# Performance work log

Hardware: AMD Instinct MI355X
Metric: run time of the kernel (lower is better)

The kernel has to match this reference:

```python
import jax, jax.numpy as jnp
import numpy as np

EPS = 1e-5


def setup_inputs() -> dict:
    key = jax.random.key(0)
    ks = jax.random.split(key, 10)
    B, C, H, W = 8, 128, 64, 64
    inputs = jax.random.normal(ks[0], (B, C, H, W), dtype=jnp.float32)
    # GroupNorm affine params
    gn_w = jnp.ones((C,), dtype=jnp.float32)
    gn_b = jnp.zeros((C,), dtype=jnp.float32)
    # Linear layers: torch nn.Linear weight is [out, in]
    s = 1.0 / np.sqrt(C)
    Wq = jax.random.uniform(ks[1], (C, C), jnp.float32, -s, s)
    bq = jax.random.uniform(ks[2], (C,), jnp.float32, -s, s)
    Wk = jax.random.uniform(ks[3], (C, C), jnp.float32, -s, s)
    bk = jax.random.uniform(ks[4], (C,), jnp.float32, -s, s)
    Wv = jax.random.uniform(ks[5], (C, C), jnp.float32, -s, s)
    bv = jax.random.uniform(ks[6], (C,), jnp.float32, -s, s)
    Wp = jax.random.uniform(ks[7], (C, C), jnp.float32, -s, s)
    bp = jax.random.uniform(ks[8], (C,), jnp.float32, -s, s)
    return {"inputs": inputs, "gn_w": gn_w, "gn_b": gn_b,
            "Wq": Wq, "bq": bq, "Wk": Wk, "bk": bk,
            "Wv": Wv, "bv": bv, "Wp": Wp, "bp": bp,
            "groups": 32}


def _group_norm(x, w, b, groups):
    B, C, H, W = x.shape
    xg = x.reshape(B, groups, C // groups, H, W)
    mu = jnp.mean(xg, axis=(2, 3, 4), keepdims=True)
    var = jnp.var(xg, axis=(2, 3, 4), keepdims=True)
    xn = ((xg - mu) * jax.lax.rsqrt(var + EPS)).reshape(B, C, H, W)
    return xn * w[None, :, None, None] + b[None, :, None, None]


def reference(inputs, gn_w, gn_b, Wq, bq, Wk, bk, Wv, bv, Wp, bp, groups):
    B, C, H, W = inputs.shape
    scale = C ** (-0.5)
    normed = _group_norm(inputs, gn_w, gn_b, groups)  # [B,C,H,W]
    x = normed.transpose(0, 2, 3, 1).reshape(B, H * W, C)  # [B,N,C] tokens
    q = x @ Wq.T + bq
    k = x @ Wk.T + bk
    v = x @ Wv.T + bv
    # full dense attention over N = H*W tokens, single head
    scores = jnp.einsum('bnc,bmc->bnm', q, k) * scale  # [B,N,N]
    attn = jax.nn.softmax(scores, axis=-1)
    out = jnp.einsum('bnm,bmc->bnc', attn, v)
    proj = out @ Wp.T + bp
    proj = proj.reshape(B, H, W, C).transpose(0, 3, 1, 2)
    return normed + proj
```

## Files before the change

### kernel.cpp

```cpp
#include <hip/hip_runtime.h>
#include <hip/hip_bf16.h>
#include <math.h>

typedef __bf16 bf16_t;
typedef __bf16 bf16x8 __attribute__((ext_vector_type(8)));
typedef float  f32x4  __attribute__((ext_vector_type(4)));
typedef float  f32x16 __attribute__((ext_vector_type(16)));

#define BB 8
#define CC 128
#define NN 4096
#define LDP 136
#define SCALE2 0.12751743342f

static __device__ __forceinline__ f32x4 mfma16(bf16x8 a, bf16x8 b, f32x4 c) {
    return __builtin_amdgcn_mfma_f32_16x16x32_bf16(a, b, c, 0, 0, 0);
}
static __device__ __forceinline__ f32x16 mfma32(bf16x8 a, bf16x8 b, f32x16 c) {
    return __builtin_amdgcn_mfma_f32_32x32x16_bf16(a, b, c, 0, 0, 0);
}
static __device__ __forceinline__ void gld16(const void* g, void* l) {
    __builtin_amdgcn_global_load_lds(
        (const __attribute__((address_space(1))) void*)g,
        (__attribute__((address_space(3))) void*)l, 16, 0, 0);
}
static __device__ __forceinline__ unsigned pack2bf(float a, float b) {
    union { bf16_t h[2]; unsigned u; } r;
    r.h[0] = (bf16_t)a; r.h[1] = (bf16_t)b;
    return r.u;
}

__global__ void __launch_bounds__(256) gn_stats(const float* __restrict__ in,
                                                float* __restrict__ stats) {
    int bg = blockIdx.x;
    const float4* p4 = (const float4*)(in + (size_t)bg * 16384);
    int tid = threadIdx.x;
    float s = 0.f, ss = 0.f;
    for (int i = tid; i < 4096; i += 256) {
        float4 v = p4[i];
        s  += v.x + v.y + v.z + v.w;
        ss += v.x*v.x + v.y*v.y + v.z*v.z + v.w*v.w;
    }
    for (int off = 1; off < 64; off <<= 1) {
        s  += __shfl_xor(s,  off, 64);
        ss += __shfl_xor(ss, off, 64);
    }
    __shared__ float red[8];
    int wv = tid >> 6;
    if ((tid & 63) == 0) { red[wv*2] = s; red[wv*2+1] = ss; }
    __syncthreads();
    if (tid == 0) {
        float S  = red[0]+red[2]+red[4]+red[6];
        float SS = red[1]+red[3]+red[5]+red[7];
        float mu  = S * (1.f/16384.f);
        float var = SS * (1.f/16384.f) - mu*mu;
        stats[bg*2]   = mu;
        stats[bg*2+1] = rsqrtf(var + 1e-5f);
    }
}

__global__ void __launch_bounds__(256) gn_apply(const float* __restrict__ in,
                                                const float* __restrict__ gw,
                                                const float* __restrict__ gb,
                                                const float* __restrict__ stats,
                                                float* __restrict__ normed,
                                                bf16_t* __restrict__ x) {
    int b  = blockIdx.x >> 6;
    int p0 = (blockIdx.x & 63) << 6;
    int tid = threadIdx.x;
    __shared__ bf16_t tile[64 * 130];
    for (int i = tid; i < 8192; i += 256) {
        int c = i >> 6, p = i & 63;
        size_t idx = ((size_t)(b*CC + c)) * NN + p0 + p;
        float v = in[idx];
        int sg = b*32 + (c >> 2);
        float xn = (v - stats[sg*2]) * stats[sg*2+1] * gw[c] + gb[c];
        normed[idx] = xn;
        tile[p*130 + c] = (bf16_t)xn;
    }
    __syncthreads();
    bf16_t* xb = x + ((size_t)(b*NN + p0)) * CC;
    for (int i = tid; i < 4096; i += 256) {
        int p = i >> 6, cp = i & 63;
        unsigned int d = *(const unsigned int*)&tile[p*130 + cp*2];
        *(unsigned int*)&xb[p*CC + cp*2] = d;
    }
}

__global__ void __launch_bounds__(256) qkv_gemm(const bf16_t* __restrict__ x,
        const float* __restrict__ Wq, const float* __restrict__ bq,
        const float* __restrict__ Wk, const float* __restrict__ bk,
        const float* __restrict__ Wv, const float* __restrict__ bv,
        bf16_t* __restrict__ q, bf16_t* __restrict__ k, bf16_t* __restrict__ vT) {
    __shared__ bf16_t wb[CC * LDP];
    const int ph  = blockIdx.x >> 8;
    const int blk = blockIdx.x & 255;
    int b  = blk >> 5;
    int n0 = (blk & 31) << 7;
    int tid = threadIdx.x;
    int lane = tid & 63, l15 = lane & 15, quad = lane >> 4;
    int w = tid >> 6;
    bf16x8 afr[2][4];
    #pragma unroll
    for (int rt = 0; rt < 2; rt++)
        #pragma unroll
        for (int kb = 0; kb < 4; kb++)
            afr[rt][kb] = *(const bf16x8*)&x[(size_t)(b*NN + n0 + w*32 + rt*16 + l15)*CC + kb*32 + quad*8];

    const float* W  = (ph == 0) ? Wq : (ph == 1 ? Wk : Wv);
    const float* bs = (ph == 0) ? bq : (ph == 1 ? bk : bv);
    for (int i = tid; i < 2048; i += 256) {
        int row = i >> 4, s8 = i & 15;
        const float* wp = W + row*128 + s8*8;
        bf16x8 v;
        #pragma unroll
        for (int j = 0; j < 8; j++) v[j] = (bf16_t)wp[j];
        *(bf16x8*)&wb[row*LDP + s8*8] = v;
    }
    __syncthreads();
    f32x4 acc[2][8];
    f32x4 z = {0.f, 0.f, 0.f, 0.f};
    #pragma unroll
    for (int rt = 0; rt < 2; rt++)
        #pragma unroll
        for (int t = 0; t < 8; t++) acc[rt][t] = z;
    #pragma unroll
    for (int kb = 0; kb < 4; kb++)
        #pragma unroll
        for (int t = 0; t < 8; t++) {
            bf16x8 bf = *(const bf16x8*)&wb[(t*16 + l15)*LDP + kb*32 + quad*8];
            acc[0][t] = mfma16(afr[0][kb], bf, acc[0][t]);
            acc[1][t] = mfma16(afr[1][kb], bf, acc[1][t]);
        }
    __syncthreads();
    if (ph < 2) {
        float sc = (ph == 0) ? SCALE2 : 1.0f;
        #pragma unroll
        for (int t = 0; t < 8; t++) {
            float bias = bs[t*16 + l15];
            #pragma unroll
            for (int rt = 0; rt < 2; rt++)
                #pragma unroll
                for (int r = 0; r < 4; r++) {
                    int nloc = w*32 + rt*16 + quad*4 + r;
                    wb[nloc*LDP + t*16 + l15] = (bf16_t)((acc[rt][t][r] + bias) * sc);
                }
        }
        __syncthreads();
        bf16_t* outp = (ph == 0) ? q : k;
        for (int i = tid; i < 2048; i += 256) {
            int row = i >> 4, g = i & 15;
            bf16x8 vv = *(const bf16x8*)&wb[row*LDP + g*8];
            int gd = (ph == 0) ? g : (g ^ (row & 15));
            *(bf16x8*)&outp[(size_t)(b*NN + n0 + row)*CC + gd*8] = vv;
        }
    } else {
        #pragma unroll
        for (int t = 0; t < 8; t++) {
            float bias = bs[t*16 + l15];
            #pragma unroll
            for (int rt = 0; rt < 2; rt++)
                #pragma unroll
                for (int r = 0; r < 4; r++) {
                    int nloc = w*32 + rt*16 + quad*4 + r;
                    wb[(t*16 + l15)*LDP + nloc] = (bf16_t)(acc[rt][t][r] + bias);
                }
        }
        __syncthreads();
        for (int i = tid; i < 8192; i += 256) {
            int c = i >> 6, np = i & 63;
            unsigned int d = *(const unsigned int*)&wb[c*LDP + np*2];
            int npp = (np & ~6) | ((np & 2) << 1) | ((np & 4) >> 1);
            int g = (npp >> 2) ^ (c & 15);
            *(unsigned int*)&vT[(size_t)(b*CC + c)*NN + n0 + (g << 3) + ((npp & 3) << 1)] = d;
        }
    }
}

__global__ void __launch_bounds__(512, 2) flash_attn(const bf16_t* __restrict__ qg_,
                                                     const bf16_t* __restrict__ kg,
                                                     const bf16_t* __restrict__ vg,
                                                     unsigned* __restrict__ opd,
                                                     float* __restrict__ mlf) {
    __shared__ bf16_t kbuf[2][128*128];
    __shared__ bf16_t vbuf[2][128*128];
    const int b    = blockIdx.x >> 5;
    const int qb   = (blockIdx.x >> 1) & 15;
    const int jh   = blockIdx.x & 1;
    const int q0   = qb << 8;
    const int j00  = jh << 11;
    const int tid  = threadIdx.x;
    const int lane = tid & 63;
    const int l31  = lane & 31;
    const int h    = lane >> 5;
    const int w    = tid >> 6;

    bf16x8 qf[8];
    {
        const bf16_t* qr = qg_ + ((size_t)(b*NN + q0 + w*32 + l31))*CC + h*8;
        #pragma unroll
        for (int kc = 0; kc < 8; kc++) qf[kc] = *(const bf16x8*)(qr + kc*16);
    }
    int gofs[8];
    #pragma unroll
    for (int kc = 0; kc < 8; kc++) gofs[kc] = ((2*kc + h) ^ (l31 & 15)) << 3;

    f32x16 ot[4];
    #pragma unroll
    for (int ct = 0; ct < 4; ct++)
        #pragma unroll
        for (int r = 0; r < 16; r++) ot[ct][r] = 0.f;
    float l = 0.f;

    {
        const bf16_t* kt = kg + ((size_t)(b*NN + j00))*CC;
        #pragma unroll
        for (int it = 0; it < 4; it++) {
            int cb = it*512 + tid;
            gld16(kt + (size_t)cb*8, &kbuf[0][cb*8]);
        }
        #pragma unroll
        for (int it = 0; it < 4; it++) {
            int c = it*512 + tid;
            gld16(vg + ((size_t)(b*CC + (c >> 4)))*NN + j00 + (c & 15)*8, &vbuf[0][c*8]);
        }
    }
    __syncthreads();

    for (int i = 0; i < 16; i++) {
        const int cur = i & 1;
        if (i < 15) {
            const int j0n = j00 + ((i + 1) << 7);
            const bf16_t* kt = kg + ((size_t)(b*NN + j0n))*CC;
            #pragma unroll
            for (int it = 0; it < 4; it++) {
                int cb = it*512 + tid;
                gld16(kt + (size_t)cb*8, &kbuf[cur^1][cb*8]);
            }
            #pragma unroll
            for (int it = 0; it < 4; it++) {
                int c = it*512 + tid;
                gld16(vg + ((size_t)(b*CC + (c >> 4)))*NN + j0n + (c & 15)*8, &vbuf[cur^1][c*8]);
            }
        }
        #pragma unroll
        for (int tt = 0; tt < 4; tt++) {
            f32x16 st;
            #pragma unroll
            for (int r = 0; r < 16; r++) st[r] = 0.f;
            const bf16_t* krow = &kbuf[cur][(tt*32 + l31)*128];
            #pragma unroll
            for (int kc = 0; kc < 8; kc++) {
                bf16x8 kf = *(const bf16x8*)(krow + gofs[kc]);
                st = mfma32(kf, qf[kc], st);
            }
            #pragma unroll
            for (int r = 0; r < 16; r++) st[r] = __builtin_amdgcn_exp2f(st[r]);
            {
                float a0 = (st[0]+st[1]) + (st[2]+st[3]);
                float a1 = (st[4]+st[5]) + (st[6]+st[7]);
                float a2 = (st[8]+st[9]) + (st[10]+st[11]);
                float a3 = (st[12]+st[13]) + (st[14]+st[15]);
                l += (a0 + a1) + (a2 + a3);
            }
            union { unsigned u[4]; bf16x8 v; } pf[2];
            #pragma unroll
            for (int kcl = 0; kcl < 2; kcl++)
                #pragma unroll
                for (int g = 0; g < 4; g++)
                    pf[kcl].u[g] = pack2bf(st[8*kcl + 2*g], st[8*kcl + 2*g + 1]);
            #pragma unroll
            for (int kcl = 0; kcl < 2; kcl++) {
                const int kc = tt*2 + kcl;
                #pragma unroll
                for (int ct = 0; ct < 4; ct++) {
                    bf16x8 vf = *(const bf16x8*)&vbuf[cur][(ct*32 + l31)*128 + gofs[kc]];
                    ot[ct] = mfma32(vf, pf[kcl].v, ot[ct]);
                }
            }
        }
        __syncthreads();
    }
    l += __shfl_xor(l, 32, 64);
    const int row0 = q0 + w*32 + l31;
    unsigned* ob = opd + ((size_t)(jh*BB + b)) * 64 * NN;
    #pragma unroll
    for (int ct = 0; ct < 4; ct++)
        #pragma unroll
        for (int rp = 0; rp < 8; rp++) {
            int cpair = ct*16 + (rp & 1) + 4*(rp >> 1) + 2*h;
            ob[(size_t)cpair*NN + row0] = pack2bf(ot[ct][2*rp], ot[ct][2*rp + 1]);
        }
    if (h == 0)
        mlf[((size_t)(jh*BB + b))*NN + row0] = l;
}

__global__ void __launch_bounds__(256) merge_attn(const unsigned* __restrict__ opd,
                                                  const float* __restrict__ mlf,
                                                  bf16_t* __restrict__ ao) {
    __shared__ float inv[128];
    __shared__ unsigned tile[128 * 65];
    const int b  = blockIdx.x >> 5;
    const int q0 = (blockIdx.x & 31) << 7;
    const int tid = threadIdx.x;
    if (tid < 128) {
        float lt = 0.f;
        #pragma unroll
        for (int p = 0; p < 2; p++) lt += mlf[((size_t)(p*BB + b))*NN + q0 + tid];
        inv[tid] = 1.0f / lt;
    }
    __syncthreads();
    for (int i = tid; i < 8192; i += 256) {
        int q = i & 127, cp = i >> 7;
        float lo = 0.f, hi = 0.f;
        #pragma unroll
        for (int p = 0; p < 2; p++) {
            unsigned u = opd[(((size_t)(p*BB + b))*64 + cp)*NN + q0 + q];
            union { unsigned u; float f; } a, c;
            a.u = u << 16; c.u = u & 0xffff0000u;
            lo += a.f; hi += c.f;
        }
        float s = inv[q];
        tile[q*65 + cp] = pack2bf(lo * s, hi * s);
    }
    __syncthreads();
    unsigned* aod = (unsigned*)ao;
    for (int i = tid; i < 8192; i += 256) {
        int q = i >> 6, cp = i & 63;
        aod[((size_t)(b*NN + q0 + q))*64 + cp] = tile[q*65 + cp];
    }
}

__global__ void __launch_bounds__(256) proj_out(const bf16_t* __restrict__ ao,
                                                const float* __restrict__ Wp,
                                                const float* __restrict__ bp,
                                                float* __restrict__ out) {
    __shared__ bf16_t wb[CC * LDP];
    int b  = blockIdx.x >> 5;
    int n0 = (blockIdx.x & 31) << 7;
    int tid = threadIdx.x;
    int lane = tid & 63, l15 = lane & 15, quad = lane >> 4;
    int w = tid >> 6;
    bf16x8 afr[2][4];
    #pragma unroll
    for (int rt = 0; rt < 2; rt++)
        #pragma unroll
        for (int kb = 0; kb < 4; kb++)
            afr[rt][kb] = *(const bf16x8*)&ao[(size_t)(b*NN + n0 + w*32 + rt*16 + l15)*CC + kb*32 + quad*8];
    for (int i = tid; i < 2048; i += 256) {
        int row = i >> 4, s8 = i & 15;
        const float* wp = Wp + row*128 + s8*8;
        bf16x8 v;
        #pragma unroll
        for (int j = 0; j < 8; j++) v[j] = (bf16_t)wp[j];
        *(bf16x8*)&wb[row*LDP + s8*8] = v;
    }
    __syncthreads();
    f32x4 acc[2][8];
    f32x4 z = {0.f, 0.f, 0.f, 0.f};
    #pragma unroll
    for (int rt = 0; rt < 2; rt++)
        #pragma unroll
        for (int t = 0; t < 8; t++) acc[rt][t] = z;
    #pragma unroll
    for (int kb = 0; kb < 4; kb++)
        #pragma unroll
        for (int t = 0; t < 8; t++) {
            bf16x8 bf = *(const bf16x8*)&wb[(t*16 + l15)*LDP + kb*32 + quad*8];
            acc[0][t] = mfma16(afr[0][kb], bf, acc[0][t]);
            acc[1][t] = mfma16(afr[1][kb], bf, acc[1][t]);
        }
    __syncthreads();
    #pragma unroll
    for (int t = 0; t < 8; t++) {
        float bias = bp[t*16 + l15];
        #pragma unroll
        for (int rt = 0; rt < 2; rt++)
            #pragma unroll
            for (int r = 0; r < 4; r++) {
                int nloc = w*32 + rt*16 + quad*4 + r;
                wb[(t*16 + l15)*LDP + nloc] = (bf16_t)(acc[rt][t][r] + bias);
            }
    }
    __syncthreads();
    for (int i = tid; i < 8192; i += 256) {
        int c = i >> 6, np = i & 63;
        bf16_t b0 = wb[c*LDP + np*2], b1 = wb[c*LDP + np*2 + 1];
        size_t idx = (size_t)(b*CC + c)*NN + n0 + np*2;
        float2 nv = *(float2*)&out[idx];
        nv.x += (float)b0;
        nv.y += (float)b1;
        *(float2*)&out[idx] = nv;
    }
}

extern "C" void kernel_launch(void* const* d_in, const int* in_sizes, int n_in,
                              void* d_out, int out_size, void* d_ws, size_t ws_size,
                              hipStream_t stream) {
    const float* in = (const float*)d_in[0];
    const float* gw = (const float*)d_in[1];
    const float* gb = (const float*)d_in[2];
    const float* Wq = (const float*)d_in[3];
    const float* bq = (const float*)d_in[4];
    const float* Wk = (const float*)d_in[5];
    const float* bk = (const float*)d_in[6];
    const float* Wv = (const float*)d_in[7];
    const float* bv = (const float*)d_in[8];
    const float* Wp = (const float*)d_in[9];
    const float* bp = (const float*)d_in[10];
    float* out = (float*)d_out;

    char* ws = (char*)d_ws;
    const size_t SZ = (size_t)BB * NN * CC * 2;
    float*    stats = (float*)ws;
    bf16_t*   x  = (bf16_t*)(ws + 2048);
    bf16_t*   q  = (bf16_t*)(ws + 2048 + SZ);
    bf16_t*   kk = (bf16_t*)(ws + 2048 + 2*SZ);
    bf16_t*   vT = (bf16_t*)(ws + 2048 + 3*SZ);
    bf16_t*   ao = (bf16_t*)(ws + 2048 + 4*SZ);
    unsigned* op = (unsigned*)(ws + 2048 + 5*SZ);
    float*    ml = (float*)(ws + 2048 + 5*SZ + (size_t)2*BB*64*NN*4);

    gn_stats  <<<256, 256, 0, stream>>>(in, stats);
    gn_apply  <<<512, 256, 0, stream>>>(in, gw, gb, stats, out, x);
    qkv_gemm  <<<768, 256, 0, stream>>>(x, Wq, bq, Wk, bk, Wv, bv, q, kk, vT);
    flash_attn<<<256, 512, 0, stream>>>(q, kk, vT, op, ml);
    merge_attn<<<256, 256, 0, stream>>>(op, ml, ao);
    proj_out  <<<256, 256, 0, stream>>>(ao, Wp, bp, out);
}
```

Baseline: 201.6 us.

## Fuse groupnorm apply into QKV GEMM, merge into projection, split KV into quarters

Group-norm application moves into the QKV GEMM, which now reads the fp32 input and builds the bf16 token tile in shared memory. The split-KV merge moves into the projection kernel, which also recomputes the normalized residual from the input. Flash attention now splits keys into four chunks of 1024 using 64-key tiles, giving 512 blocks with a launch bound allowing 4 blocks per CU. This removes two launches and the x/ao round trips through global memory. In exchange the GN math is recomputed three times (once per Q/K/V phase), and the partial-output traffic to merge doubles.

```diff
diff --git a/kernel.cpp b/kernel.cpp
--- a/kernel.cpp
+++ b/kernel.cpp
@@ -59,40 +59,14 @@
     }
 }
 
-__global__ void __launch_bounds__(256) gn_apply(const float* __restrict__ in,
-                                                const float* __restrict__ gw,
-                                                const float* __restrict__ gb,
-                                                const float* __restrict__ stats,
-                                                float* __restrict__ normed,
-                                                bf16_t* __restrict__ x) {
-    int b  = blockIdx.x >> 6;
-    int p0 = (blockIdx.x & 63) << 6;
-    int tid = threadIdx.x;
-    __shared__ bf16_t tile[64 * 130];
-    for (int i = tid; i < 8192; i += 256) {
-        int c = i >> 6, p = i & 63;
-        size_t idx = ((size_t)(b*CC + c)) * NN + p0 + p;
-        float v = in[idx];
-        int sg = b*32 + (c >> 2);
-        float xn = (v - stats[sg*2]) * stats[sg*2+1] * gw[c] + gb[c];
-        normed[idx] = xn;
-        tile[p*130 + c] = (bf16_t)xn;
-    }
-    __syncthreads();
-    bf16_t* xb = x + ((size_t)(b*NN + p0)) * CC;
-    for (int i = tid; i < 4096; i += 256) {
-        int p = i >> 6, cp = i & 63;
-        unsigned int d = *(const unsigned int*)&tile[p*130 + cp*2];
-        *(unsigned int*)&xb[p*CC + cp*2] = d;
-    }
-}
-
-__global__ void __launch_bounds__(256) qkv_gemm(const bf16_t* __restrict__ x,
+__global__ void __launch_bounds__(256) qkv_gemm(const float* __restrict__ in,
+        const float* __restrict__ stats, const float* __restrict__ gw, const float* __restrict__ gb,
         const float* __restrict__ Wq, const float* __restrict__ bq,
         const float* __restrict__ Wk, const float* __restrict__ bk,
         const float* __restrict__ Wv, const float* __restrict__ bv,
         bf16_t* __restrict__ q, bf16_t* __restrict__ k, bf16_t* __restrict__ vT) {
     __shared__ bf16_t wb[CC * LDP];
+    __shared__ bf16_t xt[128 * 130];
     const int ph  = blockIdx.x >> 8;
     const int blk = blockIdx.x & 255;
     int b  = blk >> 5;
@@ -100,13 +74,19 @@
     int tid = threadIdx.x;
     int lane = tid & 63, l15 = lane & 15, quad = lane >> 4;
     int w = tid >> 6;
-    bf16x8 afr[2][4];
-    #pragma unroll
-    for (int rt = 0; rt < 2; rt++)
-        #pragma unroll
-        for (int kb = 0; kb < 4; kb++)
-            afr[rt][kb] = *(const bf16x8*)&x[(size_t)(b*NN + n0 + w*32 + rt*16 + l15)*CC + kb*32 + quad*8];
-
+
+    for (int i = tid; i < 4096; i += 256) {
+        int c = i >> 5, p4 = i & 31;
+        const float4* inp = (const float4*)(in + (size_t)(b*CC + c)*NN + n0);
+        float4 v = inp[p4];
+        int sg = b*32 + (c >> 2);
+        float mu = stats[sg*2], rs = stats[sg*2+1];
+        float gwc = gw[c], gbc = gb[c];
+        xt[(p4*4 + 0)*130 + c] = (bf16_t)((v.x - mu)*rs*gwc + gbc);
+        xt[(p4*4 + 1)*130 + c] = (bf16_t)((v.y - mu)*rs*gwc + gbc);
+        xt[(p4*4 + 2)*130 + c] = (bf16_t)((v.z - mu)*rs*gwc + gbc);
+        xt[(p4*4 + 3)*130 + c] = (bf16_t)((v.w - mu)*rs*gwc + gbc);
+    }
     const float* W  = (ph == 0) ? Wq : (ph == 1 ? Wk : Wv);
     const float* bs = (ph == 0) ? bq : (ph == 1 ? bk : bv);
     for (int i = tid; i < 2048; i += 256) {
@@ -118,6 +98,12 @@
         *(bf16x8*)&wb[row*LDP + s8*8] = v;
     }
     __syncthreads();
+    bf16x8 afr[2][4];
+    #pragma unroll
+    for (int rt = 0; rt < 2; rt++)
+        #pragma unroll
+        for (int kb = 0; kb < 4; kb++)
+            afr[rt][kb] = *(const bf16x8*)&xt[(w*32 + rt*16 + l15)*130 + kb*32 + quad*8];
     f32x4 acc[2][8];
     f32x4 z = {0.f, 0.f, 0.f, 0.f};
     #pragma unroll
@@ -171,24 +157,26 @@
             int c = i >> 6, np = i & 63;
             unsigned int d = *(const unsigned int*)&wb[c*LDP + np*2];
             int npp = (np & ~6) | ((np & 2) << 1) | ((np & 4) >> 1);
-            int g = (npp >> 2) ^ (c & 15);
-            *(unsigned int*)&vT[(size_t)(b*CC + c)*NN + n0 + (g << 3) + ((npp & 3) << 1)] = d;
-        }
-    }
-}
-
-__global__ void __launch_bounds__(512, 2) flash_attn(const bf16_t* __restrict__ qg_,
+            int g128 = npp >> 2, s = npp & 3;
+            int jblk = g128 >> 3, g64 = g128 & 7;
+            int gs = g64 ^ (c & 7);
+            *(unsigned int*)&vT[(size_t)(b*CC + c)*NN + n0 + jblk*64 + (gs << 3) + (s << 1)] = d;
+        }
+    }
+}
+
+__global__ void __launch_bounds__(512, 4) flash_attn(const bf16_t* __restrict__ qg_,
                                                      const bf16_t* __restrict__ kg,
                                                      const bf16_t* __restrict__ vg,
                                                      unsigned* __restrict__ opd,
                                                      float* __restrict__ mlf) {
-    __shared__ bf16_t kbuf[2][128*128];
-    __shared__ bf16_t vbuf[2][128*128];
-    const int b    = blockIdx.x >> 5;
-    const int qb   = (blockIdx.x >> 1) & 15;
-    const int jh   = blockIdx.x & 1;
+    __shared__ bf16_t kbuf[2][64*128];
+    __shared__ bf16_t vbuf[2][128*64];
+    const int b    = blockIdx.x >> 6;
+    const int qb   = (blockIdx.x >> 2) & 15;
+    const int jq   = blockIdx.x & 3;
     const int q0   = qb << 8;
-    const int j00  = jh << 11;
+    const int j00  = jq << 10;
     const int tid  = threadIdx.x;
     const int lane = tid & 63;
     const int l31  = lane & 31;
@@ -201,9 +189,12 @@
         #pragma unroll
         for (int kc = 0; kc < 8; kc++) qf[kc] = *(const bf16x8*)(qr + kc*16);
     }
-    int gofs[8];
-    #pragma unroll
-    for (int kc = 0; kc < 8; kc++) gofs[kc] = ((2*kc + h) ^ (l31 & 15)) << 3;
+    int gofs16[8];
+    #pragma unroll
+    for (int kc = 0; kc < 8; kc++) gofs16[kc] = ((2*kc + h) ^ (l31 & 15)) << 3;
+    int gofs8[4];
+    #pragma unroll
+    for (int kc = 0; kc < 4; kc++) gofs8[kc] = ((2*kc + h) ^ (l31 & 7)) << 3;
 
     f32x16 ot[4];
     #pragma unroll
@@ -215,14 +206,15 @@
     {
         const bf16_t* kt = kg + ((size_t)(b*NN + j00))*CC;
         #pragma unroll
-        for (int it = 0; it < 4; it++) {
-            int cb = it*512 + tid;
-            gld16(kt + (size_t)cb*8, &kbuf[0][cb*8]);
-        }
-        #pragma unroll
-        for (int it = 0; it < 4; it++) {
-            int c = it*512 + tid;
-            gld16(vg + ((size_t)(b*CC + (c >> 4)))*NN + j00 + (c & 15)*8, &vbuf[0][c*8]);
+        for (int it = 0; it < 2; it++) {
+            int idx = it*512 + tid;
+            gld16(kt + (size_t)idx*8, &kbuf[0][idx*8]);
+        }
+        #pragma unroll
+        for (int it = 0; it < 2; it++) {
+            int idx = it*512 + tid;
+            int c = idx >> 3, g = idx & 7;
+            gld16(vg + ((size_t)(b*CC + c))*NN + j00 + g*8, &vbuf[0][idx*8]);
         }
     }
     __syncthreads();
@@ -230,28 +222,29 @@
     for (int i = 0; i < 16; i++) {
         const int cur = i & 1;
         if (i < 15) {
-            const int j0n = j00 + ((i + 1) << 7);
+            const int j0n = j00 + ((i + 1) << 6);
             const bf16_t* kt = kg + ((size_t)(b*NN + j0n))*CC;
             #pragma unroll
-            for (int it = 0; it < 4; it++) {
-                int cb = it*512 + tid;
-                gld16(kt + (size_t)cb*8, &kbuf[cur^1][cb*8]);
-            }
-            #pragma unroll
-            for (int it = 0; it < 4; it++) {
-                int c = it*512 + tid;
-                gld16(vg + ((size_t)(b*CC + (c >> 4)))*NN + j0n + (c & 15)*8, &vbuf[cur^1][c*8]);
-            }
-        }
-        #pragma unroll
-        for (int tt = 0; tt < 4; tt++) {
+            for (int it = 0; it < 2; it++) {
+                int idx = it*512 + tid;
+                gld16(kt + (size_t)idx*8, &kbuf[cur^1][idx*8]);
+            }
+            #pragma unroll
+            for (int it = 0; it < 2; it++) {
+                int idx = it*512 + tid;
+                int c = idx >> 3, g = idx & 7;
+                gld16(vg + ((size_t)(b*CC + c))*NN + j0n + g*8, &vbuf[cur^1][idx*8]);
+            }
+        }
+        #pragma unroll
+        for (int tt = 0; tt < 2; tt++) {
             f32x16 st;
             #pragma unroll
             for (int r = 0; r < 16; r++) st[r] = 0.f;
             const bf16_t* krow = &kbuf[cur][(tt*32 + l31)*128];
             #pragma unroll
             for (int kc = 0; kc < 8; kc++) {
-                bf16x8 kf = *(const bf16x8*)(krow + gofs[kc]);
+                bf16x8 kf = *(const bf16x8*)(krow + gofs16[kc]);
                 st = mfma32(kf, qf[kc], st);
             }
             #pragma unroll
@@ -274,7 +267,7 @@
                 const int kc = tt*2 + kcl;
                 #pragma unroll
                 for (int ct = 0; ct < 4; ct++) {
-                    bf16x8 vf = *(const bf16x8*)&vbuf[cur][(ct*32 + l31)*128 + gofs[kc]];
+                    bf16x8 vf = *(const bf16x8*)&vbuf[cur][(ct*32 + l31)*64 + gofs8[kc]];
                     ot[ct] = mfma32(vf, pf[kcl].v, ot[ct]);
                 }
             }
@@ -283,7 +276,7 @@
     }
     l += __shfl_xor(l, 32, 64);
     const int row0 = q0 + w*32 + l31;
-    unsigned* ob = opd + ((size_t)(jh*BB + b)) * 64 * NN;
+    unsigned* ob = opd + ((size_t)(jq*BB + b)) * 64 * NN;
     #pragma unroll
     for (int ct = 0; ct < 4; ct++)
         #pragma unroll
@@ -292,61 +285,32 @@
             ob[(size_t)cpair*NN + row0] = pack2bf(ot[ct][2*rp], ot[ct][2*rp + 1]);
         }
     if (h == 0)
-        mlf[((size_t)(jh*BB + b))*NN + row0] = l;
-}
-
-__global__ void __launch_bounds__(256) merge_attn(const unsigned* __restrict__ opd,
-                                                  const float* __restrict__ mlf,
-                                                  bf16_t* __restrict__ ao) {
-    __shared__ float inv[128];
-    __shared__ unsigned tile[128 * 65];
-    const int b  = blockIdx.x >> 5;
-    const int q0 = (blockIdx.x & 31) << 7;
-    const int tid = threadIdx.x;
-    if (tid < 128) {
-        float lt = 0.f;
-        #pragma unroll
-        for (int p = 0; p < 2; p++) lt += mlf[((size_t)(p*BB + b))*NN + q0 + tid];
-        inv[tid] = 1.0f / lt;
-    }
-    __syncthreads();
-    for (int i = tid; i < 8192; i += 256) {
-        int q = i & 127, cp = i >> 7;
-        float lo = 0.f, hi = 0.f;
-        #pragma unroll
-        for (int p = 0; p < 2; p++) {
-            unsigned u = opd[(((size_t)(p*BB + b))*64 + cp)*NN + q0 + q];
-            union { unsigned u; float f; } a, c;
-            a.u = u << 16; c.u = u & 0xffff0000u;
-            lo += a.f; hi += c.f;
-        }
-        float s = inv[q];
-        tile[q*65 + cp] = pack2bf(lo * s, hi * s);
-    }
-    __syncthreads();
-    unsigned* aod = (unsigned*)ao;
-    for (int i = tid; i < 8192; i += 256) {
-        int q = i >> 6, cp = i & 63;
-        aod[((size_t)(b*NN + q0 + q))*64 + cp] = tile[q*65 + cp];
-    }
-}
-
-__global__ void __launch_bounds__(256) proj_out(const bf16_t* __restrict__ ao,
+        mlf[((size_t)(jq*BB + b))*NN + row0] = l;
+}
+
+__global__ void __launch_bounds__(256) proj_out(const unsigned* __restrict__ opd,
+                                                const float* __restrict__ mlf,
                                                 const float* __restrict__ Wp,
                                                 const float* __restrict__ bp,
+                                                const float* __restrict__ in,
+                                                const float* __restrict__ stats,
+                                                const float* __restrict__ gw,
+                                                const float* __restrict__ gb,
                                                 float* __restrict__ out) {
     __shared__ bf16_t wb[CC * LDP];
+    __shared__ bf16_t aot[128 * 130];
+    __shared__ float invl[128];
     int b  = blockIdx.x >> 5;
     int n0 = (blockIdx.x & 31) << 7;
     int tid = threadIdx.x;
     int lane = tid & 63, l15 = lane & 15, quad = lane >> 4;
     int w = tid >> 6;
-    bf16x8 afr[2][4];
-    #pragma unroll
-    for (int rt = 0; rt < 2; rt++)
-        #pragma unroll
-        for (int kb = 0; kb < 4; kb++)
-            afr[rt][kb] = *(const bf16x8*)&ao[(size_t)(b*NN + n0 + w*32 + rt*16 + l15)*CC + kb*32 + quad*8];
+    if (tid < 128) {
+        float lt = 0.f;
+        #pragma unroll
+        for (int p = 0; p < 4; p++) lt += mlf[((size_t)(p*BB + b))*NN + n0 + tid];
+        invl[tid] = 1.0f / lt;
+    }
     for (int i = tid; i < 2048; i += 256) {
         int row = i >> 4, s8 = i & 15;
         const float* wp = Wp + row*128 + s8*8;
@@ -356,6 +320,26 @@
         *(bf16x8*)&wb[row*LDP + s8*8] = v;
     }
     __syncthreads();
+    for (int i = tid; i < 8192; i += 256) {
+        int qq = i & 127, cp = i >> 7;
+        float lo = 0.f, hi = 0.f;
+        #pragma unroll
+        for (int p = 0; p < 4; p++) {
+            unsigned u = opd[(((size_t)(p*BB + b))*64 + cp)*NN + n0 + qq];
+            union { unsigned u; float f; } a, c;
+            a.u = u << 16; c.u = u & 0xffff0000u;
+            lo += a.f; hi += c.f;
+        }
+        float s = invl[qq];
+        *(unsigned*)&aot[qq*130 + cp*2] = pack2bf(lo * s, hi * s);
+    }
+    __syncthreads();
+    bf16x8 afr[2][4];
+    #pragma unroll
+    for (int rt = 0; rt < 2; rt++)
+        #pragma unroll
+        for (int kb = 0; kb < 4; kb++)
+            afr[rt][kb] = *(const bf16x8*)&aot[(w*32 + rt*16 + l15)*130 + kb*32 + quad*8];
     f32x4 acc[2][8];
     f32x4 z = {0.f, 0.f, 0.f, 0.f};
     #pragma unroll
@@ -387,10 +371,14 @@
         int c = i >> 6, np = i & 63;
         bf16_t b0 = wb[c*LDP + np*2], b1 = wb[c*LDP + np*2 + 1];
         size_t idx = (size_t)(b*CC + c)*NN + n0 + np*2;
-        float2 nv = *(float2*)&out[idx];
-        nv.x += (float)b0;
-        nv.y += (float)b1;
-        *(float2*)&out[idx] = nv;
+        int sg = b*32 + (c >> 2);
+        float mu = stats[sg*2], rs = stats[sg*2+1];
+        float gwc = gw[c], gbc = gb[c];
+        float2 iv = *(const float2*)&in[idx];
+        float2 ov;
+        ov.x = (iv.x - mu)*rs*gwc + gbc + (float)b0;
+        ov.y = (iv.y - mu)*rs*gwc + gbc + (float)b1;
+        *(float2*)&out[idx] = ov;
     }
 }
 
@@ -413,18 +401,14 @@
     char* ws = (char*)d_ws;
     const size_t SZ = (size_t)BB * NN * CC * 2;
     float*    stats = (float*)ws;
-    bf16_t*   x  = (bf16_t*)(ws + 2048);
-    bf16_t*   q  = (bf16_t*)(ws + 2048 + SZ);
-    bf16_t*   kk = (bf16_t*)(ws + 2048 + 2*SZ);
-    bf16_t*   vT = (bf16_t*)(ws + 2048 + 3*SZ);
-    bf16_t*   ao = (bf16_t*)(ws + 2048 + 4*SZ);
-    unsigned* op = (unsigned*)(ws + 2048 + 5*SZ);
-    float*    ml = (float*)(ws + 2048 + 5*SZ + (size_t)2*BB*64*NN*4);
+    bf16_t*   q  = (bf16_t*)(ws + 2048);
+    bf16_t*   kk = (bf16_t*)(ws + 2048 + SZ);
+    bf16_t*   vT = (bf16_t*)(ws + 2048 + 2*SZ);
+    unsigned* op = (unsigned*)(ws + 2048 + 3*SZ);
+    float*    ml = (float*)(ws + 2048 + 3*SZ + (size_t)4*BB*64*NN*4);
 
     gn_stats  <<<256, 256, 0, stream>>>(in, stats);
-    gn_apply  <<<512, 256, 0, stream>>>(in, gw, gb, stats, out, x);
-    qkv_gemm  <<<768, 256, 0, stream>>>(x, Wq, bq, Wk, bk, Wv, bv, q, kk, vT);
-    flash_attn<<<256, 512, 0, stream>>>(q, kk, vT, op, ml);
-    merge_attn<<<256, 256, 0, stream>>>(op, ml, ao);
-    proj_out  <<<256, 256, 0, stream>>>(ao, Wp, bp, out);
-}
+    qkv_gemm  <<<768, 256, 0, stream>>>(in, stats, gw, gb, Wq, bq, Wk, bk, Wv, bv, q, kk, vT);
+    flash_attn<<<512, 512, 0, stream>>>(q, kk, vT, op, ml);
+    proj_out  <<<256, 256, 0, stream>>>(op, ml, Wp, bp, in, stats, gw, gb, out);
+}
```

Result: slower. 292.9 us (+45.3%).
